# Kernel tuning notes

Hardware: AMD Instinct MI355X
Metric: run time of the kernel (lower is better)

## Reference

```python
import jax, jax.numpy as jnp
import numpy as np

B, P, E = 16, 1024, 768
HID, HEADS = 768, 12
DH = HID // HEADS  # 64
EPS = 1e-5


def setup_inputs() -> dict:
    key = jax.random.key(0)
    ks = jax.random.split(key, 4)
    return {
        "x": jax.random.normal(ks[0], (B, P, E), dtype=jnp.float32),
        "ln_weight": jnp.ones((P, E), dtype=jnp.float32),
        "ln_bias": jnp.zeros((P, E), dtype=jnp.float32),
        "qkv": jax.random.normal(ks[1], (E, 3 * HID), dtype=jnp.float32),
        "lin_w": jax.random.normal(ks[2], (HID, E), dtype=jnp.float32) * 0.02,
        "lin_b": jax.random.normal(ks[3], (E,), dtype=jnp.float32) * 0.02,
    }


def reference(x, ln_weight, ln_bias, qkv, lin_w, lin_b):
    # LayerNorm over the last TWO dims (patches, emb), per torch nn.LayerNorm((P, E))
    mean = jnp.mean(x, axis=(-2, -1), keepdims=True)
    var = jnp.var(x, axis=(-2, -1), keepdims=True)
    xn = (x - mean) / jnp.sqrt(var + EPS) * ln_weight + ln_bias

    # QKV projection: [B,P,E] @ [E,3*HID] -> [B,P,3*HID]
    proj = xn @ qkv
    # view(B,P,heads,-1) then permute -> [B,heads,P,3*DH]; chunk along last dim
    proj = proj.reshape(B, P, HEADS, 3 * DH).transpose(0, 2, 1, 3)
    q, k, v = proj[..., :DH], proj[..., DH:2 * DH], proj[..., 2 * DH:]

    # Softmax-free attention: (Q K^T) V
    atten = jnp.einsum("bhqd,bhkd->bhqk", q, k)  # [B,H,P,P]
    out = jnp.einsum("bhqk,bhkd->bhqd", atten, v)  # [B,H,P,DH]

    out = out.transpose(0, 2, 1, 3).reshape(B, P, HID)
    # dropout p=0.0 (eval) -> identity
    out = jax.nn.relu(out @ lin_w + lin_b)
    return out + x
```

## Files before the change

kernel.cpp:

```cpp
#include <hip/hip_runtime.h>
#include <hip/hip_bf16.h>
#include <cstdint>

#define BB   16
#define PP   1024
#define EE   768
#define HID  768
#define NH   12
#define DH   64
#define NPB  (PP * EE)
#define MROWS (BB * PP)

typedef __bf16 bf16_t;
typedef __bf16 bf16x8 __attribute__((ext_vector_type(8)));
typedef float  f32x4  __attribute__((ext_vector_type(4)));

__device__ __forceinline__ void gld16(const void* g, void* l) {
    __builtin_amdgcn_global_load_lds(
        (const __attribute__((address_space(1))) void*)(uintptr_t)g,
        (__attribute__((address_space(3))) void*)(uint32_t)(uintptr_t)l,
        16, 0, 0);
}

__global__ __launch_bounds__(256) void stats1_kernel(const float* __restrict__ x,
                                                     float* __restrict__ part) {
    int bid = blockIdx.x;
    int b = bid >> 6, s = bid & 63;
    const float4* xp = (const float4*)(x + (size_t)b * NPB + (size_t)s * 12288);
    float sum = 0.f, ss = 0.f;
#pragma unroll
    for (int i = 0; i < 12; ++i) {
        float4 v = xp[i * 256 + threadIdx.x];
        sum += v.x + v.y + v.z + v.w;
        ss  += v.x * v.x + v.y * v.y + v.z * v.z + v.w * v.w;
    }
#pragma unroll
    for (int off = 32; off > 0; off >>= 1) {
        sum += __shfl_down(sum, off, 64);
        ss  += __shfl_down(ss,  off, 64);
    }
    __shared__ float tmp[8];
    int wave = threadIdx.x >> 6, lane = threadIdx.x & 63;
    if (lane == 0) { tmp[wave * 2] = sum; tmp[wave * 2 + 1] = ss; }
    __syncthreads();
    if (threadIdx.x == 0) {
        part[bid * 2]     = tmp[0] + tmp[2] + tmp[4] + tmp[6];
        part[bid * 2 + 1] = tmp[1] + tmp[3] + tmp[5] + tmp[7];
    }
}

__global__ __launch_bounds__(256) void prep_kernel(const float* __restrict__ qkvw,
                                                   const float* __restrict__ linw,
                                                   const float* __restrict__ part,
                                                   bf16_t* __restrict__ qkvT,
                                                   bf16_t* __restrict__ lwT,
                                                   float* __restrict__ stats) {
    int bid = blockIdx.x;
    if (bid < 576) {
        __shared__ float lds[64][65];
        const float* src; bf16_t* dst; int r0, c0, W;
        if (bid < 432) {
            int tr = bid / 36, tc = bid - tr * 36;
            r0 = tr * 64; c0 = tc * 64; src = qkvw; W = 2304; dst = qkvT;
        } else {
            int bb = bid - 432;
            int tr = bb / 12, tc = bb - tr * 12;
            r0 = tr * 64; c0 = tc * 64; src = linw; W = 768; dst = lwT;
        }
        int t = threadIdx.x;
        int rr = t >> 4, cc4 = (t & 15) * 4;
#pragma unroll
        for (int j = 0; j < 4; ++j) {
            float4 v = *(const float4*)(src + (size_t)(r0 + rr + j * 16) * W + c0 + cc4);
            lds[rr + j * 16][cc4 + 0] = v.x;
            lds[rr + j * 16][cc4 + 1] = v.y;
            lds[rr + j * 16][cc4 + 2] = v.z;
            lds[rr + j * 16][cc4 + 3] = v.w;
        }
        __syncthreads();
        int cl = t >> 3, rgl = (t & 7) * 8;
#pragma unroll
        for (int jj = 0; jj < 2; ++jj) {
            int c = jj * 32 + cl;
            union { bf16_t h[8]; uint4 u; } o;
#pragma unroll
            for (int k = 0; k < 8; ++k) o.h[k] = (bf16_t)lds[rgl + k][c];
            *(uint4*)(dst + (size_t)(c0 + c) * 768 + r0 + rgl) = o.u;
        }
    } else {
        int wave = threadIdx.x >> 6, lane = threadIdx.x & 63;
#pragma unroll
        for (int j = 0; j < 4; ++j) {
            int b = wave * 4 + j;
            float sum = part[(b * 64 + lane) * 2];
            float ss  = part[(b * 64 + lane) * 2 + 1];
#pragma unroll
            for (int off = 32; off > 0; off >>= 1) {
                sum += __shfl_down(sum, off, 64);
                ss  += __shfl_down(ss,  off, 64);
            }
            if (lane == 0) {
                const float inv_n = 1.f / (float)NPB;
                float mean = sum * inv_n;
                float var  = ss * inv_n - mean * mean;
                stats[b * 2]     = mean;
                stats[b * 2 + 1] = rsqrtf(var + 1e-5f);
            }
        }
    }
}

__global__ __launch_bounds__(256) void ln_apply_kernel(const float* __restrict__ x,
                                                       const float* __restrict__ lnw,
                                                       const float* __restrict__ lnb,
                                                       const float* __restrict__ stats,
                                                       bf16_t* __restrict__ xn) {
    int i = (blockIdx.x * 256 + threadIdx.x) * 8;
    int b = i / NPB;
    int r = i - b * NPB;
    float mean = stats[b * 2], rstd = stats[b * 2 + 1];
    float4 x0 = *(const float4*)(x + i),     x1 = *(const float4*)(x + i + 4);
    float4 w0 = *(const float4*)(lnw + r),   w1 = *(const float4*)(lnw + r + 4);
    float4 c0 = *(const float4*)(lnb + r),   c1 = *(const float4*)(lnb + r + 4);
    union { bf16_t h[8]; uint4 u; } o;
    o.h[0] = (bf16_t)((x0.x - mean) * rstd * w0.x + c0.x);
    o.h[1] = (bf16_t)((x0.y - mean) * rstd * w0.y + c0.y);
    o.h[2] = (bf16_t)((x0.z - mean) * rstd * w0.z + c0.z);
    o.h[3] = (bf16_t)((x0.w - mean) * rstd * w0.w + c0.w);
    o.h[4] = (bf16_t)((x1.x - mean) * rstd * w1.x + c1.x);
    o.h[5] = (bf16_t)((x1.y - mean) * rstd * w1.y + c1.y);
    o.h[6] = (bf16_t)((x1.z - mean) * rstd * w1.z + c1.z);
    o.h[7] = (bf16_t)((x1.w - mean) * rstd * w1.w + c1.w);
    *(uint4*)(xn + i) = o.u;
}

template <int KDIM>
__device__ __forceinline__ void gemm_core_128(const bf16_t* __restrict__ A,
                                              const bf16_t* __restrict__ Bt,
                                              int mBase, int nBase,
                                              f32x4 acc[4][4],
                                              bf16_t* As, bf16_t* Bs) {
    const int t = threadIdx.x;
    const int lane = t & 63, wave = t >> 6;
    const int wm = wave >> 1, wn = wave & 1;
    const int m16 = lane & 15, quad = lane >> 4;

    const int sr = t >> 3, s8 = t & 7;
    const bf16_t* pa[4]; const bf16_t* pb[4];
#pragma unroll
    for (int i = 0; i < 4; ++i) {
        int row = i * 32 + sr;
        int g = (s8 - (row & 7)) & 7;
        pa[i] = A  + (size_t)(mBase + row) * KDIM + g * 8;
        pb[i] = Bt + (size_t)(nBase + row) * KDIM + g * 8;
    }

    int raOff[4][2], rbOff[4][2];
#pragma unroll
    for (int i = 0; i < 4; ++i) {
        int ra = wm * 64 + i * 16 + m16;
        int rb = wn * 64 + i * 16 + m16;
#pragma unroll
        for (int ks = 0; ks < 2; ++ks) {
            raOff[i][ks] = ra * 64 + (((ks * 4 + quad) + (ra & 7)) & 7) * 8;
            rbOff[i][ks] = rb * 64 + (((ks * 4 + quad) + (rb & 7)) & 7) * 8;
        }
    }

    const f32x4 z = {0.f, 0.f, 0.f, 0.f};
#pragma unroll
    for (int mm = 0; mm < 4; ++mm)
#pragma unroll
        for (int nn = 0; nn < 4; ++nn) acc[mm][nn] = z;

    for (int k0 = 0; k0 < KDIM; k0 += 64) {
        __syncthreads();
#pragma unroll
        for (int i = 0; i < 4; ++i) {
            gld16(pa[i] + k0, As + i * 2048 + t * 8);
            gld16(pb[i] + k0, Bs + i * 2048 + t * 8);
        }
        __syncthreads();
#pragma unroll
        for (int ks = 0; ks < 2; ++ks) {
            bf16x8 af[4], bfv[4];
#pragma unroll
            for (int i = 0; i < 4; ++i) {
                af[i]  = *(const bf16x8*)(As + raOff[i][ks]);
                bfv[i] = *(const bf16x8*)(Bs + rbOff[i][ks]);
            }
#pragma unroll
            for (int mm = 0; mm < 4; ++mm)
#pragma unroll
                for (int nn = 0; nn < 4; ++nn)
                    acc[mm][nn] = __builtin_amdgcn_mfma_f32_16x16x32_bf16(
                        af[mm], bfv[nn], acc[mm][nn], 0, 0, 0);
        }
    }
}

__global__ __launch_bounds__(256, 2) void gemm_qkv_kernel(const bf16_t* __restrict__ xn,
                                                          const bf16_t* __restrict__ qkvT,
                                                          bf16_t* __restrict__ q,
                                                          bf16_t* __restrict__ kt,
                                                          bf16_t* __restrict__ vt) {
    __shared__ bf16_t smem[36864];
    const int t = threadIdx.x, lane = t & 63, wave = t >> 6;
    const int wm = wave >> 1, wn = wave & 1;
    const int m16 = lane & 15, quad = lane >> 4;

    const int lb = blockIdx.y * 9 + blockIdx.x;
    const int id = (lb & 7) * 144 + (lb >> 3);
    const int tx = id % 9, ty = id / 9;
    const int mBase = ty * 128, nBase = tx * 256;

    const bf16_t* gsrc[6];
    int ldst[6];
#pragma unroll
    for (int j = 0; j < 2; ++j) {
        int c = t + 256 * j;
        int l = c >> 3, lg = ((c & 7) - (l & 7)) & 7;
        gsrc[j] = xn + (size_t)(mBase + l + (lg >> 2) * 64) * 768 + (lg & 3) * 8;
        ldst[j] = c * 8;
    }
#pragma unroll
    for (int j = 0; j < 4; ++j) {
        int c = t + 256 * j;
        int l = c >> 3, lg = ((c & 7) - (l & 7)) & 7;
        gsrc[2 + j] = qkvT + (size_t)(nBase + l + (lg >> 2) * 128) * 768 + (lg & 3) * 8;
        ldst[2 + j] = 4096 + c * 8;
    }

    int aOff[4], bOff[8];
#pragma unroll
    for (int mf = 0; mf < 4; ++mf)
        aOff[mf] = (mf * 16 + m16) * 64 + (((wm * 4 + quad) + (m16 & 7)) & 7) * 8;
#pragma unroll
    for (int nf = 0; nf < 8; ++nf)
        bOff[nf] = 4096 + (nf * 16 + m16) * 64 + (((wn * 4 + quad) + (m16 & 7)) & 7) * 8;

    f32x4 acc[4][8];
    const f32x4 z = {0.f, 0.f, 0.f, 0.f};
#pragma unroll
    for (int mf = 0; mf < 4; ++mf)
#pragma unroll
        for (int nf = 0; nf < 8; ++nf) acc[mf][nf] = z;

#pragma unroll
    for (int j = 0; j < 6; ++j) gld16(gsrc[j], smem + ldst[j]);
#pragma unroll
    for (int j = 0; j < 6; ++j) gld16(gsrc[j] + 32, smem + 12288 + ldst[j]);

#pragma unroll
    for (int step = 0; step < 24; ++step) {
        const int cur = (step % 3) * 12288;
        asm volatile("s_waitcnt lgkmcnt(0)" ::: "memory");
        __builtin_amdgcn_sched_barrier(0);
        __builtin_amdgcn_s_barrier();
        if (step + 2 < 24) {
            const int nb = ((step + 2) % 3) * 12288;
            const int kq = (step + 2) * 32;
#pragma unroll
            for (int j = 0; j < 6; ++j)
                gld16(gsrc[j] + kq, smem + nb + ldst[j]);
        }
        if (step < 22)       asm volatile("s_waitcnt vmcnt(12)" ::: "memory");
        else if (step == 22) asm volatile("s_waitcnt vmcnt(6)"  ::: "memory");
        else                 asm volatile("s_waitcnt vmcnt(0)"  ::: "memory");
        __builtin_amdgcn_sched_barrier(0);
        __builtin_amdgcn_s_barrier();

        bf16x8 af[4], bf0[4], bf1[4];
#pragma unroll
        for (int mf = 0; mf < 4; ++mf)
            af[mf] = *(const bf16x8*)(smem + cur + aOff[mf]);
#pragma unroll
        for (int nf = 0; nf < 4; ++nf)
            bf0[nf] = *(const bf16x8*)(smem + cur + bOff[nf]);
        __builtin_amdgcn_s_setprio(1);
#pragma unroll
        for (int mf = 0; mf < 4; ++mf)
#pragma unroll
            for (int nf = 0; nf < 4; ++nf)
                acc[mf][nf] = __builtin_amdgcn_mfma_f32_16x16x32_bf16(
                    af[mf], bf0[nf], acc[mf][nf], 0, 0, 0);
        __builtin_amdgcn_s_setprio(0);
        __builtin_amdgcn_s_barrier();
#pragma unroll
        for (int nf = 0; nf < 4; ++nf)
            bf1[nf] = *(const bf16x8*)(smem + cur + bOff[4 + nf]);
        __builtin_amdgcn_s_setprio(1);
#pragma unroll
        for (int mf = 0; mf < 4; ++mf)
#pragma unroll
            for (int nf = 0; nf < 4; ++nf)
                acc[mf][4 + nf] = __builtin_amdgcn_mfma_f32_16x16x32_bf16(
                    af[mf], bf1[nf], acc[mf][4 + nf], 0, 0, 0);
        __builtin_amdgcn_s_setprio(0);
    }

    asm volatile("s_waitcnt lgkmcnt(0)" ::: "memory");
    __builtin_amdgcn_sched_barrier(0);
    bf16_t* slot = smem + wave * 4608;
    const int b = mBase >> 10, p0 = mBase & 1023;

#pragma unroll
    for (int half = 0; half < 2; ++half) {
        const int g64 = tx * 4 + wn * 2 + half;
        const int cls = g64 % 3, h = g64 / 3;
        if (cls == 0) {
#pragma unroll
            for (int mf = 0; mf < 4; ++mf)
#pragma unroll
                for (int nfl = 0; nfl < 4; ++nfl)
#pragma unroll
                    for (int i = 0; i < 4; ++i)
                        slot[(mf * 16 + quad * 4 + i) * 72 + nfl * 16 + m16] =
                            (bf16_t)acc[mf][half * 4 + nfl][i];
            asm volatile("s_waitcnt lgkmcnt(0)" ::: "memory");
            __builtin_amdgcn_sched_barrier(0);
#pragma unroll
            for (int j = 0; j < 8; ++j) {
                int r = j * 8 + (lane >> 3), cc = lane & 7;
                bf16x8 val = *(const bf16x8*)(slot + r * 72 + cc * 8);
                *(bf16x8*)(q + ((size_t)(b * 1024 + p0 + wm * 64 + r)) * 768 +
                           h * 64 + cc * 8) = val;
            }
        } else {
            bf16_t* dst = (cls == 1) ? kt : vt;
            const size_t bh = (size_t)(b * 12 + h);
#pragma unroll
            for (int mf = 0; mf < 4; ++mf)
#pragma unroll
                for (int nfl = 0; nfl < 4; ++nfl) {
                    int c = nfl * 16 + m16;
                    union { bf16_t hh[4]; uint2 u; } pk;
#pragma unroll
                    for (int i = 0; i < 4; ++i)
                        pk.hh[i] = (bf16_t)acc[mf][half * 4 + nfl][i];
                    *(uint2*)(slot + c * 72 + mf * 16 + quad * 4) = pk.u;
                }
            asm volatile("s_waitcnt lgkmcnt(0)" ::: "memory");
            __builtin_amdgcn_sched_barrier(0);
#pragma unroll
            for (int j = 0; j < 8; ++j) {
                int c = (lane >> 3) + j * 8, r8 = (lane & 7) * 8;
                bf16x8 val = *(const bf16x8*)(slot + c * 72 + r8);
                *(bf16x8*)(dst + (bh * 64 + c) * 1024 + p0 + wm * 64 + r8) = val;
            }
        }
        if (half == 0) {
            asm volatile("s_waitcnt lgkmcnt(0)" ::: "memory");
            __builtin_amdgcn_sched_barrier(0);
        }
    }
}

__global__ __launch_bounds__(256) void kv_kernel(const bf16_t* __restrict__ kt,
                                                 const bf16_t* __restrict__ vt,
                                                 bf16_t* __restrict__ thi,
                                                 bf16_t* __restrict__ tlo) {
    __shared__ float red[4 * 64 * 65];
    const int bh = blockIdx.x;
    const bf16_t* Kb = kt + (size_t)bh * DH * PP;
    const bf16_t* Vb = vt + (size_t)bh * DH * PP;
    const int t = threadIdx.x;
    const int lane = t & 63, wave = t >> 6;
    const int m16 = lane & 15, quad = lane >> 4;
    const f32x4 z = {0.f, 0.f, 0.f, 0.f};
    f32x4 acc[4][4];
#pragma unroll
    for (int mm = 0; mm < 4; ++mm)
#pragma unroll
        for (int nn = 0; nn < 4; ++nn) acc[mm][nn] = z;

    for (int ks = 0; ks < 8; ++ks) {
        int kb = wave * 256 + ks * 32 + quad * 8;
        bf16x8 af[4], bfv[4];
#pragma unroll
        for (int mm = 0; mm < 4; ++mm)
            af[mm] = *(const bf16x8*)(Kb + (size_t)(mm * 16 + m16) * PP + kb);
#pragma unroll
        for (int nn = 0; nn < 4; ++nn)
            bfv[nn] = *(const bf16x8*)(Vb + (size_t)(nn * 16 + m16) * PP + kb);
#pragma unroll
        for (int mm = 0; mm < 4; ++mm)
#pragma unroll
            for (int nn = 0; nn < 4; ++nn)
                acc[mm][nn] = __builtin_amdgcn_mfma_f32_16x16x32_bf16(
                    af[mm], bfv[nn], acc[mm][nn], 0, 0, 0);
    }
#pragma unroll
    for (int mm = 0; mm < 4; ++mm)
#pragma unroll
        for (int nn = 0; nn < 4; ++nn)
#pragma unroll
            for (int i = 0; i < 4; ++i)
                red[wave * 4160 + (mm * 16 + quad * 4 + i) * 65 + nn * 16 + m16] =
                    acc[mm][nn][i];
    __syncthreads();
#pragma unroll
    for (int j = 0; j < 16; ++j) {
        int idx = j * 256 + t;
        int m = idx >> 6, n = idx & 63;
        int a = m * 65 + n;
        float s = red[a] + red[4160 + a] + red[8320 + a] + red[12480 + a];
        bf16_t hi = (bf16_t)s;
        float lo = s - (float)hi;
        thi[(size_t)bh * 4096 + idx] = hi;
        tlo[(size_t)bh * 4096 + idx] = (bf16_t)lo;
    }
}

__global__ __launch_bounds__(256) void u_kernel(const bf16_t* __restrict__ thi,
                                                const bf16_t* __restrict__ tlo,
                                                const bf16_t* __restrict__ lwT,
                                                bf16_t* __restrict__ ut) {
    const int bh = blockIdx.x;
    const int b = bh / NH, h = bh - b * NH;
    const int nBase = blockIdx.y * 256;
    const bf16_t* Th = thi + (size_t)bh * 4096;
    const bf16_t* Tl = tlo + (size_t)bh * 4096;
    const int t = threadIdx.x, lane = t & 63, wave = t >> 6;
    const int wm = wave >> 1, wn = wave & 1;
    const int m16 = lane & 15, quad = lane >> 4;
    const f32x4 z = {0.f, 0.f, 0.f, 0.f};
    f32x4 acc[2][8];
#pragma unroll
    for (int mm = 0; mm < 2; ++mm)
#pragma unroll
        for (int nn = 0; nn < 8; ++nn) acc[mm][nn] = z;

#pragma unroll
    for (int ks = 0; ks < 2; ++ks) {
        bf16x8 ah[2], al[2], bfr[8];
#pragma unroll
        for (int mm = 0; mm < 2; ++mm) {
            ah[mm] = *(const bf16x8*)(Th + (wm * 32 + mm * 16 + m16) * 64 + ks * 32 + quad * 8);
            al[mm] = *(const bf16x8*)(Tl + (wm * 32 + mm * 16 + m16) * 64 + ks * 32 + quad * 8);
        }
#pragma unroll
        for (int nn = 0; nn < 8; ++nn)
            bfr[nn] = *(const bf16x8*)(
                lwT + (size_t)(nBase + wn * 128 + nn * 16 + m16) * 768 + h * 64 + ks * 32 + quad * 8);
#pragma unroll
        for (int mm = 0; mm < 2; ++mm)
#pragma unroll
            for (int nn = 0; nn < 8; ++nn) {
                acc[mm][nn] = __builtin_amdgcn_mfma_f32_16x16x32_bf16(
                    ah[mm], bfr[nn], acc[mm][nn], 0, 0, 0);
                acc[mm][nn] = __builtin_amdgcn_mfma_f32_16x16x32_bf16(
                    al[mm], bfr[nn], acc[mm][nn], 0, 0, 0);
            }
    }
#pragma unroll
    for (int mm = 0; mm < 2; ++mm)
#pragma unroll
        for (int nn = 0; nn < 8; ++nn) {
            int e  = nBase + wn * 128 + nn * 16 + m16;
            int d1 = wm * 32 + mm * 16 + quad * 4;
            union { bf16_t hh[4]; uint2 u; } pk;
#pragma unroll
            for (int i = 0; i < 4; ++i) pk.hh[i] = (bf16_t)acc[mm][nn][i];
            *(uint2*)(ut + ((size_t)b * 768 + e) * 768 + h * 64 + d1) = pk.u;
        }
}

__global__ __launch_bounds__(256) void gemm_out_kernel(const bf16_t* __restrict__ q,
                                                       const bf16_t* __restrict__ ut,
                                                       const float* __restrict__ linb,
                                                       const float* __restrict__ x,
                                                       float* __restrict__ out) {
    __shared__ bf16_t smem[16384];
    f32x4 acc[4][4];
    const int lb  = blockIdx.y * 6 + blockIdx.x;
    const int swz = (lb & 7) * 96 + (lb >> 3);
    const int tx  = swz % 6, ty = swz / 6;
    const int mBase = ty * 128, nBase = tx * 128;
    const int b = mBase >> 10;
    gemm_core_128<768>(q, ut + (size_t)b * 768 * 768, mBase, nBase, acc,
                       smem, smem + 8192);

    const int lane = threadIdx.x & 63, wave = threadIdx.x >> 6;
    const int wm = wave >> 1, wn = wave & 1;
    const int m16 = lane & 15, quad = lane >> 4;
#pragma unroll
    for (int mm = 0; mm < 4; ++mm) {
#pragma unroll
        for (int i = 0; i < 4; ++i) {
            size_t row = mBase + wm * 64 + mm * 16 + quad * 4 + i;
#pragma unroll
            for (int nn = 0; nn < 4; ++nn) {
                int col = nBase + wn * 64 + nn * 16 + m16;
                float v = acc[mm][nn][i] + linb[col];
                v = fmaxf(v, 0.f) + x[row * EE + col];
                out[row * EE + col] = v;
            }
        }
    }
}

extern "C" void kernel_launch(void* const* d_in, const int* in_sizes, int n_in,
                              void* d_out, int out_size, void* d_ws, size_t ws_size,
                              hipStream_t stream) {
    const float* x    = (const float*)d_in[0];
    const float* lnw  = (const float*)d_in[1];
    const float* lnb  = (const float*)d_in[2];
    const float* qkvw = (const float*)d_in[3];
    const float* linw = (const float*)d_in[4];
    const float* linb = (const float*)d_in[5];
    float* out = (float*)d_out;
    char* ws = (char*)d_ws;

    float*  part  = (float*)(ws + 0);
    float*  stats = (float*)(ws + 8192);
    bf16_t* xn    = (bf16_t*)(ws + 8448);
    bf16_t* qkvT  = (bf16_t*)(ws + 25174272);
    bf16_t* lwT   = (bf16_t*)(ws + 28713216);
    bf16_t* q     = (bf16_t*)(ws + 29892864);
    bf16_t* kt    = (bf16_t*)(ws + 55058688);
    bf16_t* vt    = (bf16_t*)(ws + 80224512);
    bf16_t* thi   = qkvT;
    bf16_t* tlo   = qkvT + 192 * 4096;
    bf16_t* ut    = kt;

    stats1_kernel<<<dim3(BB * 64), dim3(256), 0, stream>>>(x, part);
    prep_kernel<<<dim3(577), dim3(256), 0, stream>>>(qkvw, linw, part, qkvT, lwT, stats);
    ln_apply_kernel<<<dim3(6144), dim3(256), 0, stream>>>(x, lnw, lnb, stats, xn);
    gemm_qkv_kernel<<<dim3(9, 128), dim3(256), 0, stream>>>(xn, qkvT, q, kt, vt);
    kv_kernel<<<dim3(192), dim3(256), 0, stream>>>(kt, vt, thi, tlo);
    u_kernel<<<dim3(192, 3), dim3(256), 0, stream>>>(thi, tlo, lwT, ut);
    gemm_out_kernel<<<dim3(6, 128), dim3(256), 0, stream>>>(q, ut, linb, x, out);
}
```

Measured before the change: 257.1 us.

## Fuse kv and u kernels, shrink QKV tile, share pipelined core with output GEMM

```diff
diff --git a/kernel.cpp b/kernel.cpp
--- a/kernel.cpp
+++ b/kernel.cpp
@@ -134,352 +134,266 @@
     *(uint4*)(xn + i) = o.u;
 }
 
-template <int KDIM>
-__device__ __forceinline__ void gemm_core_128(const bf16_t* __restrict__ A,
-                                              const bf16_t* __restrict__ Bt,
-                                              int mBase, int nBase,
-                                              f32x4 acc[4][4],
-                                              bf16_t* As, bf16_t* Bs) {
-    const int t = threadIdx.x;
-    const int lane = t & 63, wave = t >> 6;
+__device__ __forceinline__ void core128_bk32(const bf16_t* __restrict__ A,
+                                             const bf16_t* __restrict__ Bt,
+                                             int mBase, int nBase,
+                                             f32x4 acc[4][4], bf16_t* smem) {
+    const int t = threadIdx.x, lane = t & 63, wave = t >> 6;
     const int wm = wave >> 1, wn = wave & 1;
     const int m16 = lane & 15, quad = lane >> 4;
 
-    const int sr = t >> 3, s8 = t & 7;
-    const bf16_t* pa[4]; const bf16_t* pb[4];
-#pragma unroll
-    for (int i = 0; i < 4; ++i) {
-        int row = i * 32 + sr;
-        int g = (s8 - (row & 7)) & 7;
-        pa[i] = A  + (size_t)(mBase + row) * KDIM + g * 8;
-        pb[i] = Bt + (size_t)(nBase + row) * KDIM + g * 8;
-    }
-
-    int raOff[4][2], rbOff[4][2];
-#pragma unroll
-    for (int i = 0; i < 4; ++i) {
-        int ra = wm * 64 + i * 16 + m16;
-        int rb = wn * 64 + i * 16 + m16;
-#pragma unroll
-        for (int ks = 0; ks < 2; ++ks) {
-            raOff[i][ks] = ra * 64 + (((ks * 4 + quad) + (ra & 7)) & 7) * 8;
-            rbOff[i][ks] = rb * 64 + (((ks * 4 + quad) + (rb & 7)) & 7) * 8;
-        }
+    const bf16_t* gsrc[4];
+    int ldst[4];
+#pragma unroll
+    for (int j = 0; j < 2; ++j) {
+        int c = t + 256 * j;
+        int l = c >> 3, lg = ((c & 7) - (l & 7)) & 7;
+        int row = l + (lg >> 2) * 64, kc = lg & 3;
+        gsrc[j]     = A  + (size_t)(mBase + row) * 768 + kc * 8;
+        ldst[j]     = c * 8;
+        gsrc[2 + j] = Bt + (size_t)(nBase + row) * 768 + kc * 8;
+        ldst[2 + j] = 4096 + c * 8;
+    }
+
+    int aOff[4], bOff[4];
+#pragma unroll
+    for (int f = 0; f < 4; ++f) {
+        aOff[f] = (f * 16 + m16) * 64 + (((wm * 4 + quad) + (m16 & 7)) & 7) * 8;
+        bOff[f] = 4096 + (f * 16 + m16) * 64 + (((wn * 4 + quad) + (m16 & 7)) & 7) * 8;
     }
 
     const f32x4 z = {0.f, 0.f, 0.f, 0.f};
 #pragma unroll
-    for (int mm = 0; mm < 4; ++mm)
-#pragma unroll
-        for (int nn = 0; nn < 4; ++nn) acc[mm][nn] = z;
-
-    for (int k0 = 0; k0 < KDIM; k0 += 64) {
-        __syncthreads();
-#pragma unroll
-        for (int i = 0; i < 4; ++i) {
-            gld16(pa[i] + k0, As + i * 2048 + t * 8);
-            gld16(pb[i] + k0, Bs + i * 2048 + t * 8);
-        }
-        __syncthreads();
-#pragma unroll
-        for (int ks = 0; ks < 2; ++ks) {
-            bf16x8 af[4], bfv[4];
-#pragma unroll
-            for (int i = 0; i < 4; ++i) {
-                af[i]  = *(const bf16x8*)(As + raOff[i][ks]);
-                bfv[i] = *(const bf16x8*)(Bs + rbOff[i][ks]);
-            }
-#pragma unroll
-            for (int mm = 0; mm < 4; ++mm)
-#pragma unroll
-                for (int nn = 0; nn < 4; ++nn)
-                    acc[mm][nn] = __builtin_amdgcn_mfma_f32_16x16x32_bf16(
-                        af[mm], bfv[nn], acc[mm][nn], 0, 0, 0);
-        }
-    }
-}
-
-__global__ __launch_bounds__(256, 2) void gemm_qkv_kernel(const bf16_t* __restrict__ xn,
+    for (int mf = 0; mf < 4; ++mf)
+#pragma unroll
+        for (int nf = 0; nf < 4; ++nf) acc[mf][nf] = z;
+
+#pragma unroll
+    for (int j = 0; j < 4; ++j) gld16(gsrc[j], smem + ldst[j]);
+#pragma unroll
+    for (int j = 0; j < 4; ++j) gld16(gsrc[j] + 32, smem + 8192 + ldst[j]);
+
+#pragma unroll
+    for (int step = 0; step < 24; ++step) {
+        const int cur = (step % 3) * 8192;
+        asm volatile("s_waitcnt lgkmcnt(0)" ::: "memory");
+        __builtin_amdgcn_sched_barrier(0);
+        __builtin_amdgcn_s_barrier();
+        if (step + 2 < 24) {
+            const int nb = ((step + 2) % 3) * 8192;
+            const int kq = (step + 2) * 32;
+#pragma unroll
+            for (int j = 0; j < 4; ++j)
+                gld16(gsrc[j] + kq, smem + nb + ldst[j]);
+        }
+        if (step < 22)       asm volatile("s_waitcnt vmcnt(8)" ::: "memory");
+        else if (step == 22) asm volatile("s_waitcnt vmcnt(4)" ::: "memory");
+        else                 asm volatile("s_waitcnt vmcnt(0)" ::: "memory");
+        __builtin_amdgcn_sched_barrier(0);
+        __builtin_amdgcn_s_barrier();
+
+        bf16x8 af[4], bfv[4];
+#pragma unroll
+        for (int f = 0; f < 4; ++f) {
+            af[f]  = *(const bf16x8*)(smem + cur + aOff[f]);
+            bfv[f] = *(const bf16x8*)(smem + cur + bOff[f]);
+        }
+        __builtin_amdgcn_s_setprio(1);
+#pragma unroll
+        for (int mf = 0; mf < 4; ++mf)
+#pragma unroll
+            for (int nf = 0; nf < 4; ++nf)
+                acc[mf][nf] = __builtin_amdgcn_mfma_f32_16x16x32_bf16(
+                    af[mf], bfv[nf], acc[mf][nf], 0, 0, 0);
+        __builtin_amdgcn_s_setprio(0);
+    }
+}
+
+__global__ __launch_bounds__(256, 3) void gemm_qkv_kernel(const bf16_t* __restrict__ xn,
                                                           const bf16_t* __restrict__ qkvT,
                                                           bf16_t* __restrict__ q,
                                                           bf16_t* __restrict__ kt,
                                                           bf16_t* __restrict__ vt) {
-    __shared__ bf16_t smem[36864];
+    __shared__ bf16_t smem[24576];
     const int t = threadIdx.x, lane = t & 63, wave = t >> 6;
     const int wm = wave >> 1, wn = wave & 1;
     const int m16 = lane & 15, quad = lane >> 4;
 
-    const int lb = blockIdx.y * 9 + blockIdx.x;
-    const int id = (lb & 7) * 144 + (lb >> 3);
-    const int tx = id % 9, ty = id / 9;
-    const int mBase = ty * 128, nBase = tx * 256;
-
-    const bf16_t* gsrc[6];
-    int ldst[6];
-#pragma unroll
-    for (int j = 0; j < 2; ++j) {
-        int c = t + 256 * j;
-        int l = c >> 3, lg = ((c & 7) - (l & 7)) & 7;
-        gsrc[j] = xn + (size_t)(mBase + l + (lg >> 2) * 64) * 768 + (lg & 3) * 8;
-        ldst[j] = c * 8;
-    }
-#pragma unroll
-    for (int j = 0; j < 4; ++j) {
-        int c = t + 256 * j;
-        int l = c >> 3, lg = ((c & 7) - (l & 7)) & 7;
-        gsrc[2 + j] = qkvT + (size_t)(nBase + l + (lg >> 2) * 128) * 768 + (lg & 3) * 8;
-        ldst[2 + j] = 4096 + c * 8;
-    }
-
-    int aOff[4], bOff[8];
-#pragma unroll
-    for (int mf = 0; mf < 4; ++mf)
-        aOff[mf] = (mf * 16 + m16) * 64 + (((wm * 4 + quad) + (m16 & 7)) & 7) * 8;
-#pragma unroll
-    for (int nf = 0; nf < 8; ++nf)
-        bOff[nf] = 4096 + (nf * 16 + m16) * 64 + (((wn * 4 + quad) + (m16 & 7)) & 7) * 8;
-
-    f32x4 acc[4][8];
-    const f32x4 z = {0.f, 0.f, 0.f, 0.f};
-#pragma unroll
-    for (int mf = 0; mf < 4; ++mf)
-#pragma unroll
-        for (int nf = 0; nf < 8; ++nf) acc[mf][nf] = z;
-
-#pragma unroll
-    for (int j = 0; j < 6; ++j) gld16(gsrc[j], smem + ldst[j]);
-#pragma unroll
-    for (int j = 0; j < 6; ++j) gld16(gsrc[j] + 32, smem + 12288 + ldst[j]);
-
-#pragma unroll
-    for (int step = 0; step < 24; ++step) {
-        const int cur = (step % 3) * 12288;
+    const int lb = blockIdx.y * 18 + blockIdx.x;
+    const int id = (lb & 7) * 288 + (lb >> 3);
+    const int tx = id % 18, ty = id / 18;
+    const int mBase = ty * 128, nBase = tx * 128;
+
+    f32x4 acc[4][4];
+    core128_bk32(xn, qkvT, mBase, nBase, acc, smem);
+
+    __syncthreads();
+    bf16_t* slot = smem + wave * 4608;
+    const int b = mBase >> 10, p0 = mBase & 1023;
+    const int g64 = tx * 2 + wn;
+    const int cls = g64 % 3, h = g64 / 3;
+
+    if (cls == 0) {
+#pragma unroll
+        for (int mf = 0; mf < 4; ++mf)
+#pragma unroll
+            for (int nf = 0; nf < 4; ++nf)
+#pragma unroll
+                for (int i = 0; i < 4; ++i)
+                    slot[(mf * 16 + quad * 4 + i) * 72 + nf * 16 + m16] =
+                        (bf16_t)acc[mf][nf][i];
         asm volatile("s_waitcnt lgkmcnt(0)" ::: "memory");
         __builtin_amdgcn_sched_barrier(0);
-        __builtin_amdgcn_s_barrier();
-        if (step + 2 < 24) {
-            const int nb = ((step + 2) % 3) * 12288;
-            const int kq = (step + 2) * 32;
-#pragma unroll
-            for (int j = 0; j < 6; ++j)
-                gld16(gsrc[j] + kq, smem + nb + ldst[j]);
-        }
-        if (step < 22)       asm volatile("s_waitcnt vmcnt(12)" ::: "memory");
-        else if (step == 22) asm volatile("s_waitcnt vmcnt(6)"  ::: "memory");
-        else                 asm volatile("s_waitcnt vmcnt(0)"  ::: "memory");
+#pragma unroll
+        for (int j = 0; j < 8; ++j) {
+            int r = j * 8 + (lane >> 3), cc = lane & 7;
+            bf16x8 val = *(const bf16x8*)(slot + r * 72 + cc * 8);
+            *(bf16x8*)(q + ((size_t)(b * 1024 + p0 + wm * 64 + r)) * 768 +
+                       h * 64 + cc * 8) = val;
+        }
+    } else {
+        bf16_t* dst = (cls == 1) ? kt : vt;
+        const size_t bh = (size_t)(b * 12 + h);
+#pragma unroll
+        for (int mf = 0; mf < 4; ++mf)
+#pragma unroll
+            for (int nf = 0; nf < 4; ++nf) {
+                int c = nf * 16 + m16;
+                union { bf16_t hh[4]; uint2 u; } pk;
+#pragma unroll
+                for (int i = 0; i < 4; ++i) pk.hh[i] = (bf16_t)acc[mf][nf][i];
+                *(uint2*)(slot + c * 72 + mf * 16 + quad * 4) = pk.u;
+            }
+        asm volatile("s_waitcnt lgkmcnt(0)" ::: "memory");
         __builtin_amdgcn_sched_barrier(0);
-        __builtin_amdgcn_s_barrier();
-
-        bf16x8 af[4], bf0[4], bf1[4];
-#pragma unroll
-        for (int mf = 0; mf < 4; ++mf)
-            af[mf] = *(const bf16x8*)(smem + cur + aOff[mf]);
-#pragma unroll
-        for (int nf = 0; nf < 4; ++nf)
-            bf0[nf] = *(const bf16x8*)(smem + cur + bOff[nf]);
-        __builtin_amdgcn_s_setprio(1);
-#pragma unroll
-        for (int mf = 0; mf < 4; ++mf)
-#pragma unroll
-            for (int nf = 0; nf < 4; ++nf)
-                acc[mf][nf] = __builtin_amdgcn_mfma_f32_16x16x32_bf16(
-                    af[mf], bf0[nf], acc[mf][nf], 0, 0, 0);
-        __builtin_amdgcn_s_setprio(0);
-        __builtin_amdgcn_s_barrier();
-#pragma unroll
-        for (int nf = 0; nf < 4; ++nf)
-            bf1[nf] = *(const bf16x8*)(smem + cur + bOff[4 + nf]);
-        __builtin_amdgcn_s_setprio(1);
-#pragma unroll
-        for (int mf = 0; mf < 4; ++mf)
-#pragma unroll
-            for (int nf = 0; nf < 4; ++nf)
-                acc[mf][4 + nf] = __builtin_amdgcn_mfma_f32_16x16x32_bf16(
-                    af[mf], bf1[nf], acc[mf][4 + nf], 0, 0, 0);
-        __builtin_amdgcn_s_setprio(0);
-    }
-
-    asm volatile("s_waitcnt lgkmcnt(0)" ::: "memory");
-    __builtin_amdgcn_sched_barrier(0);
-    bf16_t* slot = smem + wave * 4608;
-    const int b = mBase >> 10, p0 = mBase & 1023;
-
-#pragma unroll
-    for (int half = 0; half < 2; ++half) {
-        const int g64 = tx * 4 + wn * 2 + half;
-        const int cls = g64 % 3, h = g64 / 3;
-        if (cls == 0) {
-#pragma unroll
-            for (int mf = 0; mf < 4; ++mf)
-#pragma unroll
-                for (int nfl = 0; nfl < 4; ++nfl)
-#pragma unroll
-                    for (int i = 0; i < 4; ++i)
-                        slot[(mf * 16 + quad * 4 + i) * 72 + nfl * 16 + m16] =
-                            (bf16_t)acc[mf][half * 4 + nfl][i];
-            asm volatile("s_waitcnt lgkmcnt(0)" ::: "memory");
-            __builtin_amdgcn_sched_barrier(0);
-#pragma unroll
-            for (int j = 0; j < 8; ++j) {
-                int r = j * 8 + (lane >> 3), cc = lane & 7;
-                bf16x8 val = *(const bf16x8*)(slot + r * 72 + cc * 8);
-                *(bf16x8*)(q + ((size_t)(b * 1024 + p0 + wm * 64 + r)) * 768 +
-                           h * 64 + cc * 8) = val;
-            }
-        } else {
-            bf16_t* dst = (cls == 1) ? kt : vt;
-            const size_t bh = (size_t)(b * 12 + h);
-#pragma unroll
-            for (int mf = 0; mf < 4; ++mf)
-#pragma unroll
-                for (int nfl = 0; nfl < 4; ++nfl) {
-                    int c = nfl * 16 + m16;
-                    union { bf16_t hh[4]; uint2 u; } pk;
-#pragma unroll
-                    for (int i = 0; i < 4; ++i)
-                        pk.hh[i] = (bf16_t)acc[mf][half * 4 + nfl][i];
-                    *(uint2*)(slot + c * 72 + mf * 16 + quad * 4) = pk.u;
-                }
-            asm volatile("s_waitcnt lgkmcnt(0)" ::: "memory");
-            __builtin_amdgcn_sched_barrier(0);
-#pragma unroll
-            for (int j = 0; j < 8; ++j) {
-                int c = (lane >> 3) + j * 8, r8 = (lane & 7) * 8;
-                bf16x8 val = *(const bf16x8*)(slot + c * 72 + r8);
-                *(bf16x8*)(dst + (bh * 64 + c) * 1024 + p0 + wm * 64 + r8) = val;
-            }
-        }
-        if (half == 0) {
-            asm volatile("s_waitcnt lgkmcnt(0)" ::: "memory");
-            __builtin_amdgcn_sched_barrier(0);
-        }
-    }
-}
-
-__global__ __launch_bounds__(256) void kv_kernel(const bf16_t* __restrict__ kt,
-                                                 const bf16_t* __restrict__ vt,
-                                                 bf16_t* __restrict__ thi,
-                                                 bf16_t* __restrict__ tlo) {
+#pragma unroll
+        for (int j = 0; j < 8; ++j) {
+            int c = (lane >> 3) + j * 8, r8 = (lane & 7) * 8;
+            bf16x8 val = *(const bf16x8*)(slot + c * 72 + r8);
+            *(bf16x8*)(dst + (bh * 64 + c) * 1024 + p0 + wm * 64 + r8) = val;
+        }
+    }
+}
+
+__global__ __launch_bounds__(256) void kvu_kernel(const bf16_t* __restrict__ kt,
+                                                  const bf16_t* __restrict__ vt,
+                                                  const bf16_t* __restrict__ lwT,
+                                                  bf16_t* __restrict__ ut) {
     __shared__ float red[4 * 64 * 65];
     const int bh = blockIdx.x;
+    const int b = bh / NH, h = bh - b * NH;
     const bf16_t* Kb = kt + (size_t)bh * DH * PP;
     const bf16_t* Vb = vt + (size_t)bh * DH * PP;
     const int t = threadIdx.x;
     const int lane = t & 63, wave = t >> 6;
     const int m16 = lane & 15, quad = lane >> 4;
     const f32x4 z = {0.f, 0.f, 0.f, 0.f};
-    f32x4 acc[4][4];
-#pragma unroll
-    for (int mm = 0; mm < 4; ++mm)
-#pragma unroll
-        for (int nn = 0; nn < 4; ++nn) acc[mm][nn] = z;
-
-    for (int ks = 0; ks < 8; ++ks) {
-        int kb = wave * 256 + ks * 32 + quad * 8;
-        bf16x8 af[4], bfv[4];
+
+    {
+        f32x4 acc[4][4];
 #pragma unroll
         for (int mm = 0; mm < 4; ++mm)
-            af[mm] = *(const bf16x8*)(Kb + (size_t)(mm * 16 + m16) * PP + kb);
-#pragma unroll
-        for (int nn = 0; nn < 4; ++nn)
-            bfv[nn] = *(const bf16x8*)(Vb + (size_t)(nn * 16 + m16) * PP + kb);
+#pragma unroll
+            for (int nn = 0; nn < 4; ++nn) acc[mm][nn] = z;
+        for (int ks = 0; ks < 8; ++ks) {
+            int kb = wave * 256 + ks * 32 + quad * 8;
+            bf16x8 af[4], bfv[4];
+#pragma unroll
+            for (int mm = 0; mm < 4; ++mm)
+                af[mm] = *(const bf16x8*)(Kb + (size_t)(mm * 16 + m16) * PP + kb);
+#pragma unroll
+            for (int nn = 0; nn < 4; ++nn)
+                bfv[nn] = *(const bf16x8*)(Vb + (size_t)(nn * 16 + m16) * PP + kb);
+#pragma unroll
+            for (int mm = 0; mm < 4; ++mm)
+#pragma unroll
+                for (int nn = 0; nn < 4; ++nn)
+                    acc[mm][nn] = __builtin_amdgcn_mfma_f32_16x16x32_bf16(
+                        af[mm], bfv[nn], acc[mm][nn], 0, 0, 0);
+        }
 #pragma unroll
         for (int mm = 0; mm < 4; ++mm)
 #pragma unroll
             for (int nn = 0; nn < 4; ++nn)
-                acc[mm][nn] = __builtin_amdgcn_mfma_f32_16x16x32_bf16(
-                    af[mm], bfv[nn], acc[mm][nn], 0, 0, 0);
-    }
-#pragma unroll
-    for (int mm = 0; mm < 4; ++mm)
-#pragma unroll
-        for (int nn = 0; nn < 4; ++nn)
-#pragma unroll
-            for (int i = 0; i < 4; ++i)
-                red[wave * 4160 + (mm * 16 + quad * 4 + i) * 65 + nn * 16 + m16] =
-                    acc[mm][nn][i];
+#pragma unroll
+                for (int i = 0; i < 4; ++i)
+                    red[wave * 4160 + (mm * 16 + quad * 4 + i) * 65 + nn * 16 + m16] =
+                        acc[mm][nn][i];
+    }
     __syncthreads();
-#pragma unroll
-    for (int j = 0; j < 16; ++j) {
-        int idx = j * 256 + t;
-        int m = idx >> 6, n = idx & 63;
-        int a = m * 65 + n;
-        float s = red[a] + red[4160 + a] + red[8320 + a] + red[12480 + a];
-        bf16_t hi = (bf16_t)s;
-        float lo = s - (float)hi;
-        thi[(size_t)bh * 4096 + idx] = hi;
-        tlo[(size_t)bh * 4096 + idx] = (bf16_t)lo;
-    }
-}
-
-__global__ __launch_bounds__(256) void u_kernel(const bf16_t* __restrict__ thi,
-                                                const bf16_t* __restrict__ tlo,
-                                                const bf16_t* __restrict__ lwT,
-                                                bf16_t* __restrict__ ut) {
-    const int bh = blockIdx.x;
-    const int b = bh / NH, h = bh - b * NH;
-    const int nBase = blockIdx.y * 256;
-    const bf16_t* Th = thi + (size_t)bh * 4096;
-    const bf16_t* Tl = tlo + (size_t)bh * 4096;
-    const int t = threadIdx.x, lane = t & 63, wave = t >> 6;
+
     const int wm = wave >> 1, wn = wave & 1;
-    const int m16 = lane & 15, quad = lane >> 4;
-    const f32x4 z = {0.f, 0.f, 0.f, 0.f};
-    f32x4 acc[2][8];
+    bf16x8 ah[2][2], al[2][2];
 #pragma unroll
     for (int mm = 0; mm < 2; ++mm)
 #pragma unroll
-        for (int nn = 0; nn < 8; ++nn) acc[mm][nn] = z;
-
-#pragma unroll
-    for (int ks = 0; ks < 2; ++ks) {
-        bf16x8 ah[2], al[2], bfr[8];
-#pragma unroll
-        for (int mm = 0; mm < 2; ++mm) {
-            ah[mm] = *(const bf16x8*)(Th + (wm * 32 + mm * 16 + m16) * 64 + ks * 32 + quad * 8);
-            al[mm] = *(const bf16x8*)(Tl + (wm * 32 + mm * 16 + m16) * 64 + ks * 32 + quad * 8);
-        }
-#pragma unroll
-        for (int nn = 0; nn < 8; ++nn)
-            bfr[nn] = *(const bf16x8*)(
-                lwT + (size_t)(nBase + wn * 128 + nn * 16 + m16) * 768 + h * 64 + ks * 32 + quad * 8);
+        for (int ks = 0; ks < 2; ++ks) {
+            int d1 = wm * 32 + mm * 16 + m16;
+            int base = d1 * 65 + ks * 32 + quad * 8;
+#pragma unroll
+            for (int e = 0; e < 8; ++e) {
+                float s = red[base + e] + red[4160 + base + e] +
+                          red[8320 + base + e] + red[12480 + base + e];
+                bf16_t hi = (bf16_t)s;
+                ah[mm][ks][e] = hi;
+                al[mm][ks][e] = (bf16_t)(s - (float)hi);
+            }
+        }
+
+#pragma unroll
+    for (int ny = 0; ny < 3; ++ny) {
+        const int nBase = ny * 256;
+        f32x4 acc2[2][8];
 #pragma unroll
         for (int mm = 0; mm < 2; ++mm)
 #pragma unroll
+            for (int nn = 0; nn < 8; ++nn) acc2[mm][nn] = z;
+#pragma unroll
+        for (int ks = 0; ks < 2; ++ks) {
+            bf16x8 bfr[8];
+#pragma unroll
+            for (int nn = 0; nn < 8; ++nn)
+                bfr[nn] = *(const bf16x8*)(
+                    lwT + (size_t)(nBase + wn * 128 + nn * 16 + m16) * 768 +
+                    h * 64 + ks * 32 + quad * 8);
+#pragma unroll
+            for (int mm = 0; mm < 2; ++mm)
+#pragma unroll
+                for (int nn = 0; nn < 8; ++nn) {
+                    acc2[mm][nn] = __builtin_amdgcn_mfma_f32_16x16x32_bf16(
+                        ah[mm][ks], bfr[nn], acc2[mm][nn], 0, 0, 0);
+                    acc2[mm][nn] = __builtin_amdgcn_mfma_f32_16x16x32_bf16(
+                        al[mm][ks], bfr[nn], acc2[mm][nn], 0, 0, 0);
+                }
+        }
+#pragma unroll
+        for (int mm = 0; mm < 2; ++mm)
+#pragma unroll
             for (int nn = 0; nn < 8; ++nn) {
-                acc[mm][nn] = __builtin_amdgcn_mfma_f32_16x16x32_bf16(
-                    ah[mm], bfr[nn], acc[mm][nn], 0, 0, 0);
-                acc[mm][nn] = __builtin_amdgcn_mfma_f32_16x16x32_bf16(
-                    al[mm], bfr[nn], acc[mm][nn], 0, 0, 0);
-            }
-    }
-#pragma unroll
-    for (int mm = 0; mm < 2; ++mm)
-#pragma unroll
-        for (int nn = 0; nn < 8; ++nn) {
-            int e  = nBase + wn * 128 + nn * 16 + m16;
-            int d1 = wm * 32 + mm * 16 + quad * 4;
-            union { bf16_t hh[4]; uint2 u; } pk;
-#pragma unroll
-            for (int i = 0; i < 4; ++i) pk.hh[i] = (bf16_t)acc[mm][nn][i];
-            *(uint2*)(ut + ((size_t)b * 768 + e) * 768 + h * 64 + d1) = pk.u;
-        }
-}
-
-__global__ __launch_bounds__(256) void gemm_out_kernel(const bf16_t* __restrict__ q,
-                                                       const bf16_t* __restrict__ ut,
-                                                       const float* __restrict__ linb,
-                                                       const float* __restrict__ x,
-                                                       float* __restrict__ out) {
-    __shared__ bf16_t smem[16384];
-    f32x4 acc[4][4];
+                int e  = nBase + wn * 128 + nn * 16 + m16;
+                int d1 = wm * 32 + mm * 16 + quad * 4;
+                union { bf16_t hh[4]; uint2 u; } pk;
+#pragma unroll
+                for (int i = 0; i < 4; ++i) pk.hh[i] = (bf16_t)acc2[mm][nn][i];
+                *(uint2*)(ut + ((size_t)b * 768 + e) * 768 + h * 64 + d1) = pk.u;
+            }
+    }
+}
+
+__global__ __launch_bounds__(256, 3) void gemm_out_kernel(const bf16_t* __restrict__ q,
+                                                          const bf16_t* __restrict__ ut,
+                                                          const float* __restrict__ linb,
+                                                          const float* __restrict__ x,
+                                                          float* __restrict__ out) {
+    __shared__ bf16_t smem[24576];
     const int lb  = blockIdx.y * 6 + blockIdx.x;
     const int swz = (lb & 7) * 96 + (lb >> 3);
     const int tx  = swz % 6, ty = swz / 6;
     const int mBase = ty * 128, nBase = tx * 128;
     const int b = mBase >> 10;
-    gemm_core_128<768>(q, ut + (size_t)b * 768 * 768, mBase, nBase, acc,
-                       smem, smem + 8192);
+
+    f32x4 acc[4][4];
+    core128_bk32(q, ut + (size_t)b * 768 * 768, mBase, nBase, acc, smem);
 
     const int lane = threadIdx.x & 63, wave = threadIdx.x >> 6;
     const int wm = wave >> 1, wn = wave & 1;
@@ -520,15 +434,12 @@
     bf16_t* q     = (bf16_t*)(ws + 29892864);
     bf16_t* kt    = (bf16_t*)(ws + 55058688);
     bf16_t* vt    = (bf16_t*)(ws + 80224512);
-    bf16_t* thi   = qkvT;
-    bf16_t* tlo   = qkvT + 192 * 4096;
-    bf16_t* ut    = kt;
+    bf16_t* ut    = xn;
 
     stats1_kernel<<<dim3(BB * 64), dim3(256), 0, stream>>>(x, part);
     prep_kernel<<<dim3(577), dim3(256), 0, stream>>>(qkvw, linw, part, qkvT, lwT, stats);
     ln_apply_kernel<<<dim3(6144), dim3(256), 0, stream>>>(x, lnw, lnb, stats, xn);
-    gemm_qkv_kernel<<<dim3(9, 128), dim3(256), 0, stream>>>(xn, qkvT, q, kt, vt);
-    kv_kernel<<<dim3(192), dim3(256), 0, stream>>>(kt, vt, thi, tlo);
-    u_kernel<<<dim3(192, 3), dim3(256), 0, stream>>>(thi, tlo, lwT, ut);
+    gemm_qkv_kernel<<<dim3(18, 128), dim3(256), 0, stream>>>(xn, qkvT, q, kt, vt);
+    kvu_kernel<<<dim3(192), dim3(256), 0, stream>>>(kt, vt, lwT, ut);
     gemm_out_kernel<<<dim3(6, 128), dim3(256), 0, stream>>>(q, ut, linb, x, out);
 }
```

Measured after the change: 251.9 us. -2.0%, faster.
